# Optimization experiments

Hardware: AMD Instinct MI355X
Metric: run time of the kernel (lower is better)

Reference implementation:

```python
import jax, jax.numpy as jnp
import numpy as np

MASKED = True


def setup_inputs() -> dict:
    key = jax.random.key(0)
    kq, kk, kv = jax.random.split(key, 3)
    shape = (4, 16, 2048, 64)  # [B, H, S, d]
    q = jax.random.normal(kq, shape, dtype=jnp.float32)
    k = jax.random.normal(kk, shape, dtype=jnp.float32)
    v = jax.random.normal(kv, shape, dtype=jnp.float32)
    return {"q": q, "k": k, "v": v}


def reference(q, k, v):
    d = k.shape[-1]
    scale = 1.0 / jnp.sqrt(jnp.asarray(d, dtype=q.dtype))
    # [B, H, S, S]
    att = jnp.einsum("bhqd,bhkd->bhqk", q, k) * scale
    if MASKED:
        # Faithful to torch source: tril of the scores, then mask where zero
        tri = jnp.tril(att)
        att = jnp.where(tri == 0, -jnp.inf, att)
    att = jax.nn.softmax(att, axis=-1)
    return jnp.einsum("bhqk,bhkd->bhqd", att, v)
```

## Files before the change

### kernel.cpp

```cpp
#include <hip/hip_runtime.h>
#include <hip/hip_bf16.h>

typedef __attribute__((ext_vector_type(8)))  short bf16x8;
typedef __attribute__((ext_vector_type(4)))  float f32x4;
typedef __attribute__((ext_vector_type(16))) float f32x16;
typedef unsigned short ushort_t;

#define S_LEN 2048
#define D_DIM 64
#define FIXED_M 14.0f

#if __has_builtin(__builtin_amdgcn_exp2f)
#define EXP2(x) __builtin_amdgcn_exp2f(x)
#else
#define EXP2(x) __expf((x) * 0.6931471805599453f)
#endif

__device__ __forceinline__ short f2bf(float f) {
  union { float f; unsigned u; } x; x.f = f;
  unsigned r = x.u + 0x7fffu + ((x.u >> 16) & 1u);
  return (short)(r >> 16);
}

__device__ __forceinline__ unsigned cvtpk_bf16(float lo, float hi) {
  unsigned r;
  asm("v_cvt_pk_bf16_f32 %0, %1, %2" : "=v"(r) : "v"(lo), "v"(hi));
  return r;
}

__device__ __forceinline__ void pl32swap(unsigned& a, unsigned& b) {
  asm volatile("v_permlane32_swap_b32 %0, %1" : "+v"(a), "+v"(b));
}

__device__ __forceinline__ void gl_lds16(const ushort_t* g, ushort_t* l) {
  __builtin_amdgcn_global_load_lds(
      (const __attribute__((address_space(1))) unsigned*)g,
      (__attribute__((address_space(3))) unsigned*)l, 16, 0, 0);
}

__global__ void prep_kernel(const float* __restrict__ Kf, const float* __restrict__ Vf,
                            ushort_t* __restrict__ Kb, ushort_t* __restrict__ Vt) {
  if (blockIdx.x < 2048) {
    const long n8 = (long)64 * S_LEN * D_DIM / 8;
    long i = (long)blockIdx.x * blockDim.x + threadIdx.x;
    const long stride = (long)2048 * blockDim.x;
    for (; i < n8; i += stride) {
      const float4* p = (const float4*)(Kf + i * 8);
      float4 a = p[0], b = p[1];
      bf16x8 t;
      t[0]=f2bf(a.x); t[1]=f2bf(a.y); t[2]=f2bf(a.z); t[3]=f2bf(a.w);
      t[4]=f2bf(b.x); t[5]=f2bf(b.y); t[6]=f2bf(b.z); t[7]=f2bf(b.w);
      *(bf16x8*)(Kb + i * 8) = t;
    }
  } else {
    const int bid = blockIdx.x - 2048;
    const int h  = bid >> 5;
    const int s0 = (bid & 31) * 64;
    const float* Vh = Vf + (size_t)h * S_LEN * D_DIM;
    ushort_t* Vth   = Vt + (size_t)h * D_DIM * S_LEN;
    __shared__ float tile[64][65];
    const int r  = threadIdx.x >> 2;
    const int c4 = (threadIdx.x & 3) * 16;
#pragma unroll
    for (int j = 0; j < 16; j += 4) {
      float4 x = *(const float4*)(Vh + (size_t)(s0 + r) * D_DIM + c4 + j);
      tile[r][c4 + j + 0] = x.x; tile[r][c4 + j + 1] = x.y;
      tile[r][c4 + j + 2] = x.z; tile[r][c4 + j + 3] = x.w;
    }
    __syncthreads();
    bf16x8 o0, o1;
#pragma unroll
    for (int j = 0; j < 8; ++j) o0[j] = f2bf(tile[c4 + j][r]);
#pragma unroll
    for (int j = 0; j < 8; ++j) o1[j] = f2bf(tile[c4 + 8 + j][r]);
    *(bf16x8*)(Vth + (size_t)r * S_LEN + s0 + c4)     = o0;
    *(bf16x8*)(Vth + (size_t)r * S_LEN + s0 + c4 + 8) = o1;
  }
}

__global__ __launch_bounds__(256, 2)
void flash32_kernel(const float* __restrict__ Qf, const ushort_t* __restrict__ Kb,
                    const ushort_t* __restrict__ Vt, float* __restrict__ Og) {
  const int tid = threadIdx.x;
  const int l   = tid & 63;
  const int wv  = tid >> 6;
  const int hi  = l >> 5;
  const int l31 = l & 31;
  const int l7  = l & 7;
  const int l8  = l >> 3;

  const int bid  = blockIdx.x;
  const int r6   = bid & 63;
  const int head = (r6 & 7) * 8 + (r6 >> 3);
  const int p    = bid >> 6;
  const int qhiQ = 15 - p;
  const int qloQ = p;

  const float*    Qh = Qf + (size_t)head * S_LEN * D_DIM;
  const ushort_t* Kh = Kb + (size_t)head * S_LEN * D_DIM;
  const ushort_t* Vh = Vt + (size_t)head * D_DIM * S_LEN;
  float*          Oh = Og + (size_t)head * S_LEN * D_DIM;

  __shared__ ushort_t smK[4][64 * 64];
  __shared__ ushort_t smV[4][64 * 64];

  const int swsrc = (l7 ^ l8) * 8;
  const int rb    = l31 * 64;

#define STAGE_K(T) do {                                                    \
    const int kvk_ = (T) * 64;                                             \
    ushort_t* dk_ = smK[(T) & 3];                                          \
    _Pragma("unroll")                                                      \
    for (int u_ = 0; u_ < 2; ++u_) {                                       \
      const int idx_ = wv * 2 + u_;                                        \
      const int row_ = idx_ * 8 + l8;                                      \
      gl_lds16(Kh + (size_t)(kvk_ + row_) * 64 + swsrc, dk_ + idx_ * 512); \
    }                                                                      \
  } while (0)

#define STAGE_V(T) do {                                                    \
    const int kvv_ = (T) * 64;                                             \
    ushort_t* dv_ = smV[(T) & 3];                                          \
    _Pragma("unroll")                                                      \
    for (int u_ = 0; u_ < 2; ++u_) {                                       \
      const int idx_ = wv * 2 + u_;                                        \
      const int d_ = idx_ * 8 + l8;                                        \
      gl_lds16(Vh + (size_t)d_ * S_LEN + kvv_ + swsrc, dv_ + idx_ * 512);  \
    }                                                                      \
  } while (0)

#define VMCNT0() asm volatile("s_waitcnt vmcnt(0)" ::: "memory")
#define BAR()    __builtin_amdgcn_s_barrier()

#define QKT(S0, S1, T) do {                                                \
    _Pragma("unroll")                                                      \
    for (int i = 0; i < 16; ++i) { S0[i] = -FIXED_M; S1[i] = -FIXED_M; }   \
    const ushort_t* kb_ = smK[(T) & 3];                                    \
    __builtin_amdgcn_s_setprio(1);                                         \
    _Pragma("unroll")                                                      \
    for (int ks = 0; ks < 4; ++ks) {                                       \
      const int ch = ((ks * 2 + hi) ^ l7) * 8;                             \
      bf16x8 a0 = *(const bf16x8*)(kb_ + rb + ch);                         \
      bf16x8 a1 = *(const bf16x8*)(kb_ + 2048 + rb + ch);                  \
      S0 = __builtin_amdgcn_mfma_f32_32x32x16_bf16(a0, qf[ks], S0, 0, 0, 0); \
      S1 = __builtin_amdgcn_mfma_f32_32x32x16_bf16(a1, qf[ks], S1, 0, 0, 0); \
    }                                                                      \
    __builtin_amdgcn_s_setprio(0);                                         \
  } while (0)

#define SOFTMAX(S0, S1, KV0, PW) do {                                      \
    if ((KV0) + 63 > qminw) {                                              \
      _Pragma("unroll")                                                    \
      for (int r = 0; r < 16; ++r) {                                       \
        const int crow = (r & 3) + 8 * (r >> 2) + 4 * hi;                  \
        if ((KV0) + crow > qrow)      S0[r] = -INFINITY;                   \
        if ((KV0) + 32 + crow > qrow) S1[r] = -INFINITY;                   \
      }                                                                    \
    }                                                                      \
    _Pragma("unroll")                                                      \
    for (int i = 0; i < 16; ++i) S0[i] = EXP2(S0[i]);                      \
    _Pragma("unroll")                                                      \
    for (int i = 0; i < 16; ++i) S1[i] = EXP2(S1[i]);                      \
    float b8[8];                                                           \
    _Pragma("unroll")                                                      \
    for (int i = 0; i < 8; ++i)                                            \
      b8[i] = (S0[i] + S0[i+8]) + (S1[i] + S1[i+8]);                       \
    _Pragma("unroll")                                                      \
    for (int i = 0; i < 4; ++i) b8[i] += b8[i+4];                          \
    l_run += (b8[0] + b8[2]) + (b8[1] + b8[3]);                            \
    _Pragma("unroll")                                                      \
    for (int ks = 0; ks < 4; ++ks) {                                       \
      const int r0 = (ks & 1) * 8;                                         \
      unsigned w0, w1, w2, w3;                                             \
      if (ks < 2) {                                                        \
        w0 = cvtpk_bf16(S0[r0+0], S0[r0+1]); w2 = cvtpk_bf16(S0[r0+4], S0[r0+5]); \
        w1 = cvtpk_bf16(S0[r0+2], S0[r0+3]); w3 = cvtpk_bf16(S0[r0+6], S0[r0+7]); \
      } else {                                                             \
        w0 = cvtpk_bf16(S1[r0+0], S1[r0+1]); w2 = cvtpk_bf16(S1[r0+4], S1[r0+5]); \
        w1 = cvtpk_bf16(S1[r0+2], S1[r0+3]); w3 = cvtpk_bf16(S1[r0+6], S1[r0+7]); \
      }                                                                    \
      pl32swap(w0, w2); pl32swap(w1, w3);                                  \
      union { unsigned u[4]; bf16x8 v; } pu_;                              \
      pu_.u[0] = w0; pu_.u[1] = w1; pu_.u[2] = w2; pu_.u[3] = w3;          \
      PW[ks] = pu_.v;                                                      \
    }                                                                      \
  } while (0)

#define PV(T, PW) do {                                                     \
    const ushort_t* vb_ = smV[(T) & 3];                                    \
    __builtin_amdgcn_s_setprio(1);                                         \
    _Pragma("unroll")                                                      \
    for (int ks = 0; ks < 4; ++ks) {                                       \
      const int ch = ((ks * 2 + hi) ^ l7) * 8;                             \
      bf16x8 va  = *(const bf16x8*)(vb_ + rb + ch);                        \
      bf16x8 vB2 = *(const bf16x8*)(vb_ + 2048 + rb + ch);                 \
      accA = __builtin_amdgcn_mfma_f32_32x32x16_bf16(va,  PW[ks], accA, 0, 0, 0); \
      accB = __builtin_amdgcn_mfma_f32_32x32x16_bf16(vB2, PW[ks], accB, 0, 0, 0); \
    }                                                                      \
    __builtin_amdgcn_s_setprio(0);                                         \
  } while (0)

  for (int seg = 0; seg < 2; ++seg) {
    const int qidx = seg ? qloQ : qhiQ;
    const int q0   = qidx * 128;
    const int nt   = 2 * qidx + 2;

    const int qrow  = q0 + wv * 32 + l31;
    const int qminw = q0 + wv * 32;

    STAGE_K(0);
    STAGE_V(0);
    STAGE_K(1);
    STAGE_V(1);

    bf16x8 qf[4];
    {
      const float sc = 0.125f * 1.44269504089f;
      const float* qp = Qh + (size_t)qrow * D_DIM + 8 * hi;
#pragma unroll
      for (int ks = 0; ks < 4; ++ks) {
        float4 x = *(const float4*)(qp + ks * 16);
        float4 y = *(const float4*)(qp + ks * 16 + 4);
        bf16x8 t;
        t[0]=f2bf(x.x*sc); t[1]=f2bf(x.y*sc);
        t[2]=f2bf(x.z*sc); t[3]=f2bf(x.w*sc);
        t[4]=f2bf(y.x*sc); t[5]=f2bf(y.y*sc);
        t[6]=f2bf(y.z*sc); t[7]=f2bf(y.w*sc);
        qf[ks] = t;
      }
    }

    f32x16 accA, accB, sA0, sA1, sB0, sB1;
#pragma unroll
    for (int i = 0; i < 16; ++i) { accA[i] = 0.f; accB[i] = 0.f; }
    float l_run = 0.f;
    bf16x8 pwA[4], pwB[4];

    VMCNT0();
    BAR();

    for (int t = 0; t < nt; t += 2) {
      if (t + 2 < nt) {
        STAGE_K(t + 2);
        STAGE_V(t + 2);
        STAGE_K(t + 3);
        STAGE_V(t + 3);
      }
      QKT(sA0, sA1, t);
      QKT(sB0, sB1, t + 1);
      SOFTMAX(sA0, sA1, t * 64, pwA);
      SOFTMAX(sB0, sB1, (t + 1) * 64, pwB);
      PV(t, pwA);
      PV(t + 1, pwB);
      VMCNT0();
      BAR();
    }

    l_run += __shfl_xor(l_run, 32, 64);
    const float inv = 1.0f / l_run;
    float* op = Oh + (size_t)qrow * D_DIM + 4 * hi;
#pragma unroll
    for (int m4 = 0; m4 < 4; ++m4) {
      float4 a = { accA[4*m4+0]*inv, accA[4*m4+1]*inv,
                   accA[4*m4+2]*inv, accA[4*m4+3]*inv };
      *(float4*)(op + 8 * m4) = a;
      float4 b = { accB[4*m4+0]*inv, accB[4*m4+1]*inv,
                   accB[4*m4+2]*inv, accB[4*m4+3]*inv };
      *(float4*)(op + 32 + 8 * m4) = b;
    }
  }

#undef STAGE_K
#undef STAGE_V
#undef VMCNT0
#undef BAR
#undef QKT
#undef SOFTMAX
#undef PV
}

#define BQ 64
#define BK 64
#define LDK 72
#define LDP 72

__device__ __forceinline__ unsigned pack_bf(float lo, float hi) {
  return (unsigned)(unsigned short)f2bf(lo) |
         ((unsigned)(unsigned short)f2bf(hi) << 16);
}

__global__ __launch_bounds__(256, 2)
void flash_fwd_kernel(const float* __restrict__ Qg, const float* __restrict__ Kg,
                      const float* __restrict__ Vg, float* __restrict__ Og) {
  const int tid  = threadIdx.x;
  const int lane = tid & 63;
  const int wv   = tid >> 6;
  const int grp  = lane >> 4;
  const int l16  = lane & 15;
  const int bid = blockIdx.x;
  const int qb  = 31 - (bid & 31);
  const int bh  = bid >> 5;
  const int q0  = qb * BQ;
  const size_t hoff = (size_t)bh * S_LEN * D_DIM;
  const float* Qh = Qg + hoff;
  const float* Kh = Kg + hoff;
  const float* Vh = Vg + hoff;
  float*       Oh = Og + hoff;
  __shared__ short sK [BK][LDK];
  __shared__ short sVT[D_DIM][LDP];
  __shared__ short sP [4][16][LDP];
  bf16x8 qf[2];
  {
    const float* qrow = Qh + (size_t)(q0 + wv*16 + l16) * D_DIM + grp*8;
#pragma unroll
    for (int kc = 0; kc < 2; ++kc) {
      float4 a = *reinterpret_cast<const float4*>(qrow + kc*32);
      float4 b = *reinterpret_cast<const float4*>(qrow + kc*32 + 4);
      bf16x8 t;
      t[0]=f2bf(a.x*0.125f); t[1]=f2bf(a.y*0.125f);
      t[2]=f2bf(a.z*0.125f); t[3]=f2bf(a.w*0.125f);
      t[4]=f2bf(b.x*0.125f); t[5]=f2bf(b.y*0.125f);
      t[6]=f2bf(b.z*0.125f); t[7]=f2bf(b.w*0.125f);
      qf[kc] = t;
    }
  }
  f32x4 acc[4];
#pragma unroll
  for (int nb = 0; nb < 4; ++nb) acc[nb] = (f32x4){0.f, 0.f, 0.f, 0.f};
  float m_i[4] = {-INFINITY, -INFINITY, -INFINITY, -INFINITY};
  float l_i[4] = {0.f, 0.f, 0.f, 0.f};
  const int srow = tid >> 2;
  const int scb  = tid & 3;
  for (int kt = 0; kt <= qb; ++kt) {
    const int kv0 = kt * BK;
    __syncthreads();
    {
      const float* src = Kh + (size_t)(kv0 + srow) * D_DIM + scb*16;
      float4 x0 = *reinterpret_cast<const float4*>(src);
      float4 x1 = *reinterpret_cast<const float4*>(src + 4);
      float4 x2 = *reinterpret_cast<const float4*>(src + 8);
      float4 x3 = *reinterpret_cast<const float4*>(src + 12);
      bf16x8 lo, hi;
      lo[0]=f2bf(x0.x); lo[1]=f2bf(x0.y); lo[2]=f2bf(x0.z); lo[3]=f2bf(x0.w);
      lo[4]=f2bf(x1.x); lo[5]=f2bf(x1.y); lo[6]=f2bf(x1.z); lo[7]=f2bf(x1.w);
      hi[0]=f2bf(x2.x); hi[1]=f2bf(x2.y); hi[2]=f2bf(x2.z); hi[3]=f2bf(x2.w);
      hi[4]=f2bf(x3.x); hi[5]=f2bf(x3.y); hi[6]=f2bf(x3.z); hi[7]=f2bf(x3.w);
      *reinterpret_cast<bf16x8*>(&sK[srow][scb*16])     = lo;
      *reinterpret_cast<bf16x8*>(&sK[srow][scb*16 + 8]) = hi;
    }
    {
      const float* src = Vh + (size_t)(kv0 + scb*16) * D_DIM + srow;
      bf16x8 lo, hi;
#pragma unroll
      for (int j = 0; j < 8; ++j) lo[j] = f2bf(src[(size_t)j * D_DIM]);
#pragma unroll
      for (int j = 0; j < 8; ++j) hi[j] = f2bf(src[(size_t)(j + 8) * D_DIM]);
      *reinterpret_cast<bf16x8*>(&sVT[srow][scb*16])     = lo;
      *reinterpret_cast<bf16x8*>(&sVT[srow][scb*16 + 8]) = hi;
    }
    __syncthreads();
    f32x4 sc[4];
#pragma unroll
    for (int nb = 0; nb < 4; ++nb) {
      f32x4 c = (f32x4){0.f, 0.f, 0.f, 0.f};
#pragma unroll
      for (int kc = 0; kc < 2; ++kc) {
        bf16x8 kf = *reinterpret_cast<const bf16x8*>(&sK[nb*16 + l16][kc*32 + grp*8]);
        c = __builtin_amdgcn_mfma_f32_16x16x32_bf16(qf[kc], kf, c, 0, 0, 0);
      }
      sc[nb] = c;
    }
    const bool diag = (kt == qb);
#pragma unroll
    for (int r = 0; r < 4; ++r) {
      const int qi = wv*16 + grp*4 + r;
      float s0 = sc[0][r], s1 = sc[1][r], s2 = sc[2][r], s3 = sc[3][r];
      if (diag) {
        if (l16 +  0 > qi) s0 = -INFINITY;
        if (l16 + 16 > qi) s1 = -INFINITY;
        if (l16 + 32 > qi) s2 = -INFINITY;
        if (l16 + 48 > qi) s3 = -INFINITY;
      }
      float mx = fmaxf(fmaxf(s0, s1), fmaxf(s2, s3));
#pragma unroll
      for (int off = 8; off; off >>= 1)
        mx = fmaxf(mx, __shfl_xor(mx, off, 64));
      const float mn    = fmaxf(m_i[r], mx);
      const float alpha = __expf(m_i[r] - mn);
      const float p0 = __expf(s0 - mn);
      const float p1 = __expf(s1 - mn);
      const float p2 = __expf(s2 - mn);
      const float p3 = __expf(s3 - mn);
      float rs = (p0 + p1) + (p2 + p3);
#pragma unroll
      for (int off = 8; off; off >>= 1)
        rs += __shfl_xor(rs, off, 64);
      l_i[r] = l_i[r] * alpha + rs;
      m_i[r] = mn;
      acc[0][r] *= alpha; acc[1][r] *= alpha;
      acc[2][r] *= alpha; acc[3][r] *= alpha;
      const float n0 = __shfl_xor(p0, 1, 64);
      const float n1 = __shfl_xor(p1, 1, 64);
      const float n2 = __shfl_xor(p2, 1, 64);
      const float n3 = __shfl_xor(p3, 1, 64);
      if (!(lane & 1)) {
        const int prow = grp*4 + r;
        unsigned* base = reinterpret_cast<unsigned*>(&sP[wv][prow][l16]);
        base[0]  = pack_bf(p0, n0);
        base[8]  = pack_bf(p1, n1);
        base[16] = pack_bf(p2, n2);
        base[24] = pack_bf(p3, n3);
      }
    }
    bf16x8 pf[2];
#pragma unroll
    for (int kc = 0; kc < 2; ++kc)
      pf[kc] = *reinterpret_cast<const bf16x8*>(&sP[wv][l16][kc*32 + grp*8]);
#pragma unroll
    for (int nb = 0; nb < 4; ++nb) {
#pragma unroll
      for (int kc = 0; kc < 2; ++kc) {
        bf16x8 vf = *reinterpret_cast<const bf16x8*>(&sVT[l16 + 16*nb][kc*32 + grp*8]);
        acc[nb] = __builtin_amdgcn_mfma_f32_16x16x32_bf16(pf[kc], vf, acc[nb], 0, 0, 0);
      }
    }
  }
#pragma unroll
  for (int r = 0; r < 4; ++r) {
    const float inv = 1.0f / l_i[r];
    float* orow = Oh + (size_t)(q0 + wv*16 + grp*4 + r) * D_DIM + l16;
#pragma unroll
    for (int nb = 0; nb < 4; ++nb)
      orow[nb*16] = acc[nb][r] * inv;
  }
}

extern "C" void kernel_launch(void* const* d_in, const int* in_sizes, int n_in,
                              void* d_out, int out_size, void* d_ws, size_t ws_size,
                              hipStream_t stream) {
  (void)n_in; (void)out_size;
  const float* q = (const float*)d_in[0];
  const float* k = (const float*)d_in[1];
  const float* v = (const float*)d_in[2];
  float* o = (float*)d_out;
  const int bh = in_sizes[0] / (S_LEN * D_DIM);
  const size_t elems = (size_t)bh * S_LEN * D_DIM;

  if (ws_size >= elems * 2 * 2 && bh == 64) {
    ushort_t* Kb = (ushort_t*)d_ws;
    ushort_t* Vt = Kb + elems;
    prep_kernel<<<4096, 256, 0, stream>>>(k, v, Kb, Vt);
    flash32_kernel<<<bh * 8, 256, 0, stream>>>(q, Kb, Vt, o);
  } else {
    flash_fwd_kernel<<<bh * (S_LEN / BQ), 256, 0, stream>>>(q, k, v, o);
  }
}
```

Before: 72.32 us.

## Software-pipeline attention loop: overlap QK^T of next tile with softmax/PV

Restructures the inner KV loop into a skewed pipeline. QK^T for the next tile is issued before the softmax and PV of the current tile, and K/V staging runs one tile at a time, three tiles ahead, with partial vmcnt waits and a barrier every tile instead of every two. The s_setprio raises around the MFMA blocks are removed, and a single P register buffer replaces the two. This is meant to hide global-load latency and let MFMA work overlap the exp/convert work, at the cost of twice as many barriers and tighter ordering between the 4-slot LDS ring and the vmcnt counts.

New measurement: 76.81 us. 6.2% more time.

```diff
diff --git a/kernel.cpp b/kernel.cpp
--- a/kernel.cpp
+++ b/kernel.cpp
@@ -129,14 +129,13 @@
     }                                                                      \
   } while (0)
 
-#define VMCNT0() asm volatile("s_waitcnt vmcnt(0)" ::: "memory")
+#define VMCNT(N) asm volatile("s_waitcnt vmcnt(" #N ")" ::: "memory")
 #define BAR()    __builtin_amdgcn_s_barrier()
 
 #define QKT(S0, S1, T) do {                                                \
     _Pragma("unroll")                                                      \
     for (int i = 0; i < 16; ++i) { S0[i] = -FIXED_M; S1[i] = -FIXED_M; }   \
     const ushort_t* kb_ = smK[(T) & 3];                                    \
-    __builtin_amdgcn_s_setprio(1);                                         \
     _Pragma("unroll")                                                      \
     for (int ks = 0; ks < 4; ++ks) {                                       \
       const int ch = ((ks * 2 + hi) ^ l7) * 8;                             \
@@ -145,10 +144,9 @@
       S0 = __builtin_amdgcn_mfma_f32_32x32x16_bf16(a0, qf[ks], S0, 0, 0, 0); \
       S1 = __builtin_amdgcn_mfma_f32_32x32x16_bf16(a1, qf[ks], S1, 0, 0, 0); \
     }                                                                      \
-    __builtin_amdgcn_s_setprio(0);                                         \
   } while (0)
 
-#define SOFTMAX(S0, S1, KV0, PW) do {                                      \
+#define SOFTMAX(S0, S1, KV0) do {                                          \
     if ((KV0) + 63 > qminw) {                                              \
       _Pragma("unroll")                                                    \
       for (int r = 0; r < 16; ++r) {                                       \
@@ -182,22 +180,20 @@
       pl32swap(w0, w2); pl32swap(w1, w3);                                  \
       union { unsigned u[4]; bf16x8 v; } pu_;                              \
       pu_.u[0] = w0; pu_.u[1] = w1; pu_.u[2] = w2; pu_.u[3] = w3;          \
-      PW[ks] = pu_.v;                                                      \
+      pw[ks] = pu_.v;                                                      \
     }                                                                      \
   } while (0)
 
-#define PV(T, PW) do {                                                     \
+#define PV(T) do {                                                         \
     const ushort_t* vb_ = smV[(T) & 3];                                    \
-    __builtin_amdgcn_s_setprio(1);                                         \
     _Pragma("unroll")                                                      \
     for (int ks = 0; ks < 4; ++ks) {                                       \
       const int ch = ((ks * 2 + hi) ^ l7) * 8;                             \
       bf16x8 va  = *(const bf16x8*)(vb_ + rb + ch);                        \
       bf16x8 vB2 = *(const bf16x8*)(vb_ + 2048 + rb + ch);                 \
-      accA = __builtin_amdgcn_mfma_f32_32x32x16_bf16(va,  PW[ks], accA, 0, 0, 0); \
-      accB = __builtin_amdgcn_mfma_f32_32x32x16_bf16(vB2, PW[ks], accB, 0, 0, 0); \
-    }                                                                      \
-    __builtin_amdgcn_s_setprio(0);                                         \
+      accA = __builtin_amdgcn_mfma_f32_32x32x16_bf16(va,  pw[ks], accA, 0, 0, 0); \
+      accB = __builtin_amdgcn_mfma_f32_32x32x16_bf16(vB2, pw[ks], accB, 0, 0, 0); \
+    }                                                                      \
   } while (0)
 
   for (int seg = 0; seg < 2; ++seg) {
@@ -208,10 +204,9 @@
     const int qrow  = q0 + wv * 32 + l31;
     const int qminw = q0 + wv * 32;
 
-    STAGE_K(0);
-    STAGE_V(0);
-    STAGE_K(1);
-    STAGE_V(1);
+    STAGE_K(0); STAGE_V(0);
+    STAGE_K(1); STAGE_V(1);
+    if (nt > 2) { STAGE_K(2); STAGE_V(2); }
 
     bf16x8 qf[4];
     {
@@ -234,25 +229,24 @@
 #pragma unroll
     for (int i = 0; i < 16; ++i) { accA[i] = 0.f; accB[i] = 0.f; }
     float l_run = 0.f;
-    bf16x8 pwA[4], pwB[4];
-
-    VMCNT0();
+    bf16x8 pw[4];
+
+    if (nt > 2) VMCNT(4); else VMCNT(0);
     BAR();
+    QKT(sA0, sA1, 0);
 
     for (int t = 0; t < nt; t += 2) {
-      if (t + 2 < nt) {
-        STAGE_K(t + 2);
-        STAGE_V(t + 2);
-        STAGE_K(t + 3);
-        STAGE_V(t + 3);
-      }
-      QKT(sA0, sA1, t);
+      if (t + 3 < nt) { STAGE_K(t + 3); STAGE_V(t + 3); }
       QKT(sB0, sB1, t + 1);
-      SOFTMAX(sA0, sA1, t * 64, pwA);
-      SOFTMAX(sB0, sB1, (t + 1) * 64, pwB);
-      PV(t, pwA);
-      PV(t + 1, pwB);
-      VMCNT0();
+      SOFTMAX(sA0, sA1, t * 64);
+      PV(t);
+      if (t + 3 < nt) VMCNT(4); else VMCNT(0);
+      BAR();
+      if (t + 4 < nt) { STAGE_K(t + 4); STAGE_V(t + 4); }
+      if (t + 2 < nt) QKT(sA0, sA1, t + 2);
+      SOFTMAX(sB0, sB1, (t + 1) * 64);
+      PV(t + 1);
+      if (t + 4 < nt) VMCNT(4); else VMCNT(0);
       BAR();
     }
 
@@ -272,7 +266,7 @@
 
 #undef STAGE_K
 #undef STAGE_V
-#undef VMCNT0
+#undef VMCNT
 #undef BAR
 #undef QKT
 #undef SOFTMAX
```
